# Kernel optimization log

Measured on AMD Instinct MI355X. Metric: run time of the kernel, lower is better.

The kernel has to match this reference:

```python
import jax, jax.numpy as jnp
import numpy as np

B, C, H, W, HEADS = 2, 128, 56, 56, 4
ASYM_W = 0.5


def setup_inputs() -> dict:
    key = jax.random.key(0)
    ks = jax.random.split(key, 9)
    s = lambda k, shape: jax.random.normal(k, shape, jnp.float32) * 0.02
    inner = C  # dim_head * heads == dim
    return {
        "x": jax.random.normal(ks[0], (B, C, H, W), jnp.float32),
        "Wq": s(ks[1], (inner, C)),
        "Wk": s(ks[2], (inner, C)),
        "Wv": s(ks[3], (inner, C)),
        "Wo": s(ks[4], (C, inner)),
        "bo": jnp.zeros((C,), jnp.float32),
        "Wa1": s(ks[5], (C, 2 * C)),
        "ba1": jnp.zeros((C,), jnp.float32),
        "Wa2": s(ks[6], (1, C)),
        "ba2": jnp.zeros((1,), jnp.float32),
    }


def _conv1x1(Wmat, t, bias=None):
    # 1x1 conv == per-pixel matmul over channels
    out = jnp.einsum('oc,bchw->bohw', Wmat, t)
    if bias is not None:
        out = out + bias[None, :, None, None]
    return out


def reference(x, Wq, Wk, Wv, Wo, bo, Wa1, ba1, Wa2, ba2):
    b, c, h, w = x.shape
    heads = HEADS
    dh = c // heads
    scale = dh ** -0.5

    # ---- asymmetry map ----
    left = x[:, :, :, : w // 2]
    right = x[:, :, :, w // 2:]
    right_flipped = right[:, :, :, ::-1]
    mw = min(left.shape[3], right_flipped.shape[3])
    cat = jnp.concatenate([left[:, :, :, :mw], right_flipped[:, :, :, :mw]], axis=1)
    a = _conv1x1(Wa1, cat, ba1)
    a = jax.nn.gelu(a, approximate=False)  # torch default GELU is exact erf
    a = _conv1x1(Wa2, a, ba2)
    a = jax.nn.sigmoid(a)
    # bilinear, align_corners=False == half-pixel convention of jax.image.resize
    asym = jax.image.resize(a, (b, 1, h, w), method='linear')

    # ---- q/k/v projections ----
    def heads_split(t):  # b (h d) x y -> b h (x y) d
        return t.reshape(b, heads, dh, h * w).transpose(0, 1, 3, 2)

    q = heads_split(_conv1x1(Wq, x))
    k = heads_split(_conv1x1(Wk, x))
    v = heads_split(_conv1x1(Wv, x))

    dots = jnp.einsum('bhid,bhjd->bhij', q, k) * scale  # [b,h,hw,hw]

    # 3x3 neighborhood mask, vectorized
    idx = jnp.arange(h * w)
    ii, jj = idx // w, idx % w
    mask = ((jnp.abs(ii[:, None] - ii[None, :]) <= 1)
            & (jnp.abs(jj[:, None] - jj[None, :]) <= 1)).astype(dots.dtype)
    dots = dots * mask + (1.0 - mask) * -1e9

    attn = jax.nn.softmax(dots, axis=-1)
    out = jnp.einsum('bhij,bhjd->bhid', attn, v)
    out = out.transpose(0, 1, 3, 2).reshape(b, c, h, w)  # b h (x y) d -> b (h d) x y

    out = out * (1.0 + ASYM_W * asym)
    return _conv1x1(Wo, out, bo)
```

## Files before the change

### kernel.cpp

```cpp
#include <hip/hip_runtime.h>
#include <hip/hip_bf16.h>
#include <math.h>

#define B_ 2
#define C_ 128
#define H_ 56
#define W_ 56
#define N_ (H_*W_)
#define HEADS_ 4
#define DH_ 32
#define MW_ 28
#define NPOS_ (H_*MW_)

typedef unsigned short ushort_t;
typedef __bf16 v8bf __attribute__((ext_vector_type(8)));
typedef float  v4f  __attribute__((ext_vector_type(4)));

#define MFMA16(a,b,c) __builtin_amdgcn_mfma_f32_16x16x32_bf16((a),(b),(c),0,0,0)

__device__ __forceinline__ unsigned short f2bf(float f) {
    return __builtin_bit_cast(unsigned short, __float2bfloat16(f));
}
__device__ __forceinline__ unsigned int bfpack(float a, float b) {
    return (unsigned int)f2bf(a) | ((unsigned int)f2bf(b) << 16);
}
__device__ __forceinline__ void unpack8(uint4 u, float* f) {
    f[0] = __uint_as_float(u.x << 16); f[1] = __uint_as_float(u.x & 0xffff0000u);
    f[2] = __uint_as_float(u.y << 16); f[3] = __uint_as_float(u.y & 0xffff0000u);
    f[4] = __uint_as_float(u.z << 16); f[5] = __uint_as_float(u.z & 0xffff0000u);
    f[6] = __uint_as_float(u.w << 16); f[7] = __uint_as_float(u.w & 0xffff0000u);
}

__global__ __launch_bounds__(256)
void xpose_kernel(const float* __restrict__ x, ushort_t* __restrict__ xbf) {
    __shared__ float xs[128 * 68];
    const int t  = threadIdx.x;
    const int n0 = blockIdx.x * 64;
    const int b  = blockIdx.y;
    const float* xb = x + (size_t)b * C_ * N_;

    for (int it = 0; it < 8; ++it) {
        int idx = t + it * 256;
        int c = idx >> 4, f4 = idx & 15;
        *(float4*)(&xs[c * 68 + f4 * 4]) =
            *(const float4*)(xb + (size_t)c * N_ + n0 + f4 * 4);
    }
    __syncthreads();
    const int rot = t & 7;
    for (int it = 0; it < 4; ++it) {
        int task = t + it * 256;
        int ug = task & 15, px = task >> 4;
        float f[8];
        #pragma unroll
        for (int s = 0; s < 8; ++s) {
            int u = (s + rot) & 7;
            f[u] = xs[(ug * 8 + u) * 68 + px];
        }
        uint4 o;
        o.x = bfpack(f[0], f[1]); o.y = bfpack(f[2], f[3]);
        o.z = bfpack(f[4], f[5]); o.w = bfpack(f[6], f[7]);
        *(uint4*)(xbf + ((size_t)b * N_ + n0 + px) * C_ + ug * 8) = o;
    }
}

__global__ __launch_bounds__(256)
void qkv_asym_kernel(const ushort_t* __restrict__ xbf,
                     const float* __restrict__ Wq, const float* __restrict__ Wk,
                     const float* __restrict__ Wv,
                     const float* __restrict__ Wa1, const float* __restrict__ ba1,
                     const float* __restrict__ Wa2, const float* __restrict__ ba2,
                     ushort_t* __restrict__ q, ushort_t* __restrict__ k,
                     ushort_t* __restrict__ v, float* __restrict__ aval) {
    __shared__ __align__(16) char smem[35840];
    const int t = threadIdx.x;
    const int b = blockIdx.z;
    const int wv_ = t >> 6;
    const int l   = t & 63;
    const int lr  = l & 15;
    const int lq  = l >> 4;

    if (blockIdx.y < 6) {
        ushort_t* WT = (ushort_t*)smem;
        ushort_t* XT = (ushort_t*)(smem + 17408);

        const int n0   = blockIdx.x * 64;
        const int mIdx = blockIdx.y >> 1;
        const int o0   = (blockIdx.y & 1) * 64;
        const float* W  = (mIdx == 0 ? Wq : (mIdx == 1 ? Wk : Wv));
        ushort_t* dst   = (mIdx == 0 ? q  : (mIdx == 1 ? k  : v ));

        for (int it = 0; it < 8; ++it) {
            int idx = t + it * 256;
            int row = idx >> 5, f4 = idx & 31;
            float4 w4 = *(const float4*)(W + (size_t)(o0 + row) * C_ + f4 * 4);
            ushort4 p4 = { f2bf(w4.x), f2bf(w4.y), f2bf(w4.z), f2bf(w4.w) };
            *(ushort4*)(WT + row * 136 + f4 * 4) = p4;
        }
        for (int it = 0; it < 4; ++it) {
            int idx = t + it * 256;
            int px = idx >> 4, g = idx & 15;
            uint4 r = *(const uint4*)(xbf + ((size_t)b * N_ + n0 + px) * C_ + g * 8);
            *(uint4*)(XT + px * 136 + g * 8) = r;
        }
        __syncthreads();

        v4f acc[4];
        #pragma unroll
        for (int nt = 0; nt < 4; ++nt) acc[nt] = (v4f){0.f, 0.f, 0.f, 0.f};

        #pragma unroll
        for (int ks = 0; ks < 4; ++ks) {
            v8bf af = *(const v8bf*)(WT + (wv_ * 16 + lr) * 136 + ks * 32 + lq * 8);
            #pragma unroll
            for (int nt = 0; nt < 4; ++nt) {
                v8bf bfr = *(const v8bf*)(XT + (nt * 16 + lr) * 136 + ks * 32 + lq * 8);
                acc[nt] = MFMA16(af, bfr, acc[nt]);
            }
        }

        __syncthreads();
        ushort_t* epT = WT;
        #pragma unroll
        for (int nt = 0; nt < 4; ++nt) {
            uint2 pk;
            pk.x = bfpack(acc[nt][0], acc[nt][1]);
            pk.y = bfpack(acc[nt][2], acc[nt][3]);
            *(uint2*)(epT + (nt * 16 + lr) * 136 + wv_ * 16 + lq * 4) = pk;
        }
        __syncthreads();
        for (int it = 0; it < 2; ++it) {
            int idx = t + it * 256;
            int px = idx >> 3, g = idx & 7;
            *(uint4*)(dst + ((size_t)b * N_ + n0 + px) * C_ + o0 + g * 8) =
                *(const uint4*)(epT + px * 136 + g * 8);
        }
    } else {
        ushort_t* wa  = (ushort_t*)smem;
        ushort_t* cat = (ushort_t*)(smem + 18432);
        float* wred   = (float*)(smem + 35328);

        const int P0 = blockIdx.x * 32;

        for (int it = 0; it < 4; ++it) {
            int idx = t + it * 256;
            int pos = idx >> 5, g = idx & 31;
            int pg = P0 + pos;
            int h = pg / MW_, j = pg - h * MW_;
            int n = h * W_ + ((g < 16) ? j : (W_ - 1 - j));
            uint4 r = *(const uint4*)(xbf + ((size_t)b * N_ + n) * C_ + (g & 15) * 8);
            *(uint4*)(cat + pos * 264 + g * 8) = r;
        }

        v4f acc2[2][2];
        #pragma unroll
        for (int mi = 0; mi < 2; ++mi)
            #pragma unroll
            for (int nt = 0; nt < 2; ++nt) acc2[mi][nt] = (v4f){0.f, 0.f, 0.f, 0.f};

        for (int kc = 0; kc < 4; ++kc) {
            __syncthreads();
            for (int it = 0; it < 8; ++it) {
                int idx = t + it * 256;
                int row = idx >> 4, f4 = idx & 15;
                float4 w4 = *(const float4*)(Wa1 + (size_t)row * 256 + kc * 64 + f4 * 4);
                ushort4 p4 = { f2bf(w4.x), f2bf(w4.y), f2bf(w4.z), f2bf(w4.w) };
                *(ushort4*)(wa + row * 72 + f4 * 4) = p4;
            }
            __syncthreads();
            #pragma unroll
            for (int ks = 0; ks < 2; ++ks) {
                v8bf a0f = *(const v8bf*)(wa + ((2*wv_ + 0) * 16 + lr) * 72 + ks * 32 + lq * 8);
                v8bf a1f = *(const v8bf*)(wa + ((2*wv_ + 1) * 16 + lr) * 72 + ks * 32 + lq * 8);
                v8bf b0f = *(const v8bf*)(cat + lr * 264        + kc * 64 + ks * 32 + lq * 8);
                v8bf b1f = *(const v8bf*)(cat + (16 + lr) * 264 + kc * 64 + ks * 32 + lq * 8);
                acc2[0][0] = MFMA16(a0f, b0f, acc2[0][0]);
                acc2[0][1] = MFMA16(a0f, b1f, acc2[0][1]);
                acc2[1][0] = MFMA16(a1f, b0f, acc2[1][0]);
                acc2[1][1] = MFMA16(a1f, b1f, acc2[1][1]);
            }
        }

        float p2[2] = {0.f, 0.f};
        #pragma unroll
        for (int mi = 0; mi < 2; ++mi) {
            #pragma unroll
            for (int r = 0; r < 4; ++r) {
                int m = (2*wv_ + mi) * 16 + lq * 4 + r;
                float wa2v = Wa2[m];
                float b1v  = ba1[m];
                #pragma unroll
                for (int nt = 0; nt < 2; ++nt) {
                    float val = acc2[mi][nt][r] + b1v;
                    float gl = 0.5f * val * (1.0f + erff(val * 0.7071067811865475f));
                    p2[nt] += gl * wa2v;
                }
            }
        }
        #pragma unroll
        for (int nt = 0; nt < 2; ++nt) {
            p2[nt] += __shfl_xor(p2[nt], 16, 64);
            p2[nt] += __shfl_xor(p2[nt], 32, 64);
        }
        if (l < 16) {
            wred[wv_ * 32 + lr]      = p2[0];
            wred[wv_ * 32 + 16 + lr] = p2[1];
        }
        __syncthreads();
        if (t < 32) {
            float s = wred[t] + wred[32 + t] + wred[64 + t] + wred[96 + t] + ba2[0];
            aval[(size_t)b * NPOS_ + P0 + t] = 1.0f / (1.0f + expf(-s));
        }
    }
}

__global__ __launch_bounds__(256)
void attn_oproj_kernel(const ushort_t* __restrict__ q, const ushort_t* __restrict__ k,
                       const ushort_t* __restrict__ v, const float* __restrict__ aval,
                       const float* __restrict__ Wo, const float* __restrict__ bo,
                       float* __restrict__ out) {
    __shared__ __align__(16) char smem[53248];
    ushort_t* WoT = (ushort_t*)smem;
    ushort_t* aoT = (ushort_t*)(smem + 34816);
    float*    ep  = (float*)(smem + 34816);

    const int t  = threadIdx.x;
    const int n0 = blockIdx.x * 32;
    const int b  = blockIdx.y;

    for (int it = 0; it < 16; ++it) {
        int idx = t + it * 256;
        int row = idx >> 5, f4 = idx & 31;
        float4 w4 = *(const float4*)(Wo + (size_t)row * C_ + f4 * 4);
        ushort4 p4 = { f2bf(w4.x), f2bf(w4.y), f2bf(w4.z), f2bf(w4.w) };
        *(ushort4*)(WoT + row * 136 + f4 * 4) = p4;
    }

    const size_t base = (size_t)b * N_ * C_;
    for (int u = 0; u < 2; ++u) {
        int task = t + u * 256;
        int s = task & 3, head = (task >> 2) & 3, p = task >> 4;
        int n = n0 + p;
        int i = n / W_, j = n - i * W_;
        int dbase = head * DH_ + s * 8;

        float qf[8];
        unpack8(*(const uint4*)(q + base + (size_t)n * C_ + dbase), qf);

        float dts[9]; int mm[9];
        #pragma unroll
        for (int tt = 0; tt < 9; ++tt) {
            int di = tt / 3 - 1, dj = tt % 3 - 1;
            int ii = i + di, jj = j + dj;
            bool ok = ((unsigned)ii < (unsigned)H_) && ((unsigned)jj < (unsigned)W_);
            int m = ok ? ii * W_ + jj : n;
            mm[tt] = m;
            float kf[8];
            unpack8(*(const uint4*)(k + base + (size_t)m * C_ + dbase), kf);
            float pd = qf[0]*kf[0] + qf[1]*kf[1] + qf[2]*kf[2] + qf[3]*kf[3]
                     + qf[4]*kf[4] + qf[5]*kf[5] + qf[6]*kf[6] + qf[7]*kf[7];
            pd += __shfl_xor(pd, 1, 64);
            pd += __shfl_xor(pd, 2, 64);
            dts[tt] = ok ? pd * 0.17677669529663687f : -1e30f;
        }
        float mx = dts[0];
        #pragma unroll
        for (int tt = 1; tt < 9; ++tt) mx = fmaxf(mx, dts[tt]);
        float sum = 0.f;
        #pragma unroll
        for (int tt = 0; tt < 9; ++tt) { dts[tt] = expf(dts[tt] - mx); sum += dts[tt]; }
        const float inv = 1.0f / sum;

        float acc[8] = {0,0,0,0,0,0,0,0};
        #pragma unroll
        for (int tt = 0; tt < 9; ++tt) {
            float vf[8];
            unpack8(*(const uint4*)(v + base + (size_t)mm[tt] * C_ + dbase), vf);
            float wt = dts[tt] * inv;
            #pragma unroll
            for (int d = 0; d < 8; ++d) acc[d] += wt * vf[d];
        }

        float f = 0.5f * (float)j - 0.25f;
        f = fminf(fmaxf(f, 0.0f), 27.0f);
        int i0 = (int)f; if (i0 > 26) i0 = 26;
        float frac = f - (float)i0;
        const float* av = aval + (size_t)b * NPOS_ + i * MW_;
        float a = av[i0] * (1.0f - frac) + av[i0 + 1] * frac;
        float sc = 1.0f + 0.5f * a;

        uint4 o;
        o.x = bfpack(acc[0] * sc, acc[1] * sc);
        o.y = bfpack(acc[2] * sc, acc[3] * sc);
        o.z = bfpack(acc[4] * sc, acc[5] * sc);
        o.w = bfpack(acc[6] * sc, acc[7] * sc);
        *(uint4*)(aoT + p * 136 + dbase) = o;
    }
    __syncthreads();

    const int wv_ = t >> 6, l = t & 63, lr = l & 15, lq = l >> 4;
    v4f acc4[2][2];
    #pragma unroll
    for (int mi = 0; mi < 2; ++mi)
        #pragma unroll
        for (int nt = 0; nt < 2; ++nt) acc4[mi][nt] = (v4f){0.f, 0.f, 0.f, 0.f};

    #pragma unroll
    for (int ks = 0; ks < 4; ++ks) {
        v8bf b0 = *(const v8bf*)(aoT + lr * 136        + ks * 32 + lq * 8);
        v8bf b1 = *(const v8bf*)(aoT + (16 + lr) * 136 + ks * 32 + lq * 8);
        #pragma unroll
        for (int mi = 0; mi < 2; ++mi) {
            v8bf af = *(const v8bf*)(WoT + ((wv_ * 2 + mi) * 16 + lr) * 136 + ks * 32 + lq * 8);
            acc4[mi][0] = MFMA16(af, b0, acc4[mi][0]);
            acc4[mi][1] = MFMA16(af, b1, acc4[mi][1]);
        }
    }
    __syncthreads();

    #pragma unroll
    for (int mi = 0; mi < 2; ++mi) {
        int o = (wv_ * 2 + mi) * 16 + lq * 4;
        float4 bv = *(const float4*)(bo + o);
        const float bvr[4] = { bv.x, bv.y, bv.z, bv.w };
        #pragma unroll
        for (int nt = 0; nt < 2; ++nt)
            #pragma unroll
            for (int r = 0; r < 4; ++r)
                ep[(o + r) * 36 + nt * 16 + lr] = acc4[mi][nt][r] + bvr[r];
    }
    __syncthreads();
    for (int it = 0; it < 4; ++it) {
        int idx = t + it * 256;
        int o = idx >> 3, f4 = idx & 7;
        *(float4*)(out + (size_t)b * C_ * N_ + (size_t)o * N_ + n0 + f4 * 4) =
            *(const float4*)(ep + o * 36 + f4 * 4);
    }
}

extern "C" void kernel_launch(void* const* d_in, const int* in_sizes, int n_in,
                              void* d_out, int out_size, void* d_ws, size_t ws_size,
                              hipStream_t stream) {
    const float* x   = (const float*)d_in[0];
    const float* Wq  = (const float*)d_in[1];
    const float* Wk  = (const float*)d_in[2];
    const float* Wv  = (const float*)d_in[3];
    const float* Wo  = (const float*)d_in[4];
    const float* bo  = (const float*)d_in[5];
    const float* Wa1 = (const float*)d_in[6];
    const float* ba1 = (const float*)d_in[7];
    const float* Wa2 = (const float*)d_in[8];
    const float* ba2 = (const float*)d_in[9];
    float* out = (float*)d_out;

    const size_t PXC = (size_t)B_ * N_ * C_;
    ushort_t* qb  = (ushort_t*)d_ws;
    ushort_t* kb  = qb + PXC;
    ushort_t* vb  = kb + PXC;
    ushort_t* xbf = vb + PXC;
    float*    aval = (float*)(xbf + PXC);

    xpose_kernel   <<<dim3(49, B_), 256, 0, stream>>>(x, xbf);
    qkv_asym_kernel<<<dim3(49, 7, B_), 256, 0, stream>>>(
        xbf, Wq, Wk, Wv, Wa1, ba1, Wa2, ba2, qb, kb, vb, aval);
    attn_oproj_kernel<<<dim3(98, B_), 256, 0, stream>>>(qb, kb, vb, aval, Wo, bo, out);
}
```

Before: 102.6 us.

## Fuse transpose into QKV/asym kernel and halve attention block pixel tile

```diff
diff --git a/kernel.cpp b/kernel.cpp
--- a/kernel.cpp
+++ b/kernel.cpp
@@ -32,39 +32,7 @@
 }
 
 __global__ __launch_bounds__(256)
-void xpose_kernel(const float* __restrict__ x, ushort_t* __restrict__ xbf) {
-    __shared__ float xs[128 * 68];
-    const int t  = threadIdx.x;
-    const int n0 = blockIdx.x * 64;
-    const int b  = blockIdx.y;
-    const float* xb = x + (size_t)b * C_ * N_;
-
-    for (int it = 0; it < 8; ++it) {
-        int idx = t + it * 256;
-        int c = idx >> 4, f4 = idx & 15;
-        *(float4*)(&xs[c * 68 + f4 * 4]) =
-            *(const float4*)(xb + (size_t)c * N_ + n0 + f4 * 4);
-    }
-    __syncthreads();
-    const int rot = t & 7;
-    for (int it = 0; it < 4; ++it) {
-        int task = t + it * 256;
-        int ug = task & 15, px = task >> 4;
-        float f[8];
-        #pragma unroll
-        for (int s = 0; s < 8; ++s) {
-            int u = (s + rot) & 7;
-            f[u] = xs[(ug * 8 + u) * 68 + px];
-        }
-        uint4 o;
-        o.x = bfpack(f[0], f[1]); o.y = bfpack(f[2], f[3]);
-        o.z = bfpack(f[4], f[5]); o.w = bfpack(f[6], f[7]);
-        *(uint4*)(xbf + ((size_t)b * N_ + n0 + px) * C_ + ug * 8) = o;
-    }
-}
-
-__global__ __launch_bounds__(256)
-void qkv_asym_kernel(const ushort_t* __restrict__ xbf,
+void qkv_asym_kernel(const float* __restrict__ x,
                      const float* __restrict__ Wq, const float* __restrict__ Wk,
                      const float* __restrict__ Wv,
                      const float* __restrict__ Wa1, const float* __restrict__ ba1,
@@ -88,6 +56,7 @@
         const int o0   = (blockIdx.y & 1) * 64;
         const float* W  = (mIdx == 0 ? Wq : (mIdx == 1 ? Wk : Wv));
         ushort_t* dst   = (mIdx == 0 ? q  : (mIdx == 1 ? k  : v ));
+        const float* xb = x + (size_t)b * C_ * N_;
 
         for (int it = 0; it < 8; ++it) {
             int idx = t + it * 256;
@@ -96,11 +65,18 @@
             ushort4 p4 = { f2bf(w4.x), f2bf(w4.y), f2bf(w4.z), f2bf(w4.w) };
             *(ushort4*)(WT + row * 136 + f4 * 4) = p4;
         }
-        for (int it = 0; it < 4; ++it) {
-            int idx = t + it * 256;
-            int px = idx >> 4, g = idx & 15;
-            uint4 r = *(const uint4*)(xbf + ((size_t)b * N_ + n0 + px) * C_ + g * 8);
-            *(uint4*)(XT + px * 136 + g * 8) = r;
+        {
+            int px = t & 63, g = t >> 6;
+            const float* xc = xb + n0 + px;
+            for (int it = 0; it < 8; ++it) {
+                int c0 = (g + it * 4) * 4;
+                float a0 = xc[(size_t)(c0 + 0) * N_];
+                float a1 = xc[(size_t)(c0 + 1) * N_];
+                float a2 = xc[(size_t)(c0 + 2) * N_];
+                float a3 = xc[(size_t)(c0 + 3) * N_];
+                ushort4 p4 = { f2bf(a0), f2bf(a1), f2bf(a2), f2bf(a3) };
+                *(ushort4*)(XT + px * 136 + c0) = p4;
+            }
         }
         __syncthreads();
 
@@ -140,15 +116,23 @@
         float* wred   = (float*)(smem + 35328);
 
         const int P0 = blockIdx.x * 32;
-
-        for (int it = 0; it < 4; ++it) {
-            int idx = t + it * 256;
-            int pos = idx >> 5, g = idx & 31;
+        const float* xb = x + (size_t)b * C_ * N_;
+
+        {
+            int pos = t & 31, chg = t >> 5;
             int pg = P0 + pos;
             int h = pg / MW_, j = pg - h * MW_;
-            int n = h * W_ + ((g < 16) ? j : (W_ - 1 - j));
-            uint4 r = *(const uint4*)(xbf + ((size_t)b * N_ + n) * C_ + (g & 15) * 8);
-            *(uint4*)(cat + pos * 264 + g * 8) = r;
+            int col = (chg < 4) ? (h * W_ + j) : (h * W_ + (W_ - 1 - j));
+            int cbase = (chg & 3) * 32;
+            const float* src = xb + col;
+            ushort_t* crow = cat + pos * 264 + chg * 32;
+            #pragma unroll
+            for (int u = 0; u < 16; ++u) {
+                float f0 = src[(size_t)(cbase + 2 * u) * N_];
+                float f1 = src[(size_t)(cbase + 2 * u + 1) * N_];
+                ushort2 pp = { f2bf(f0), f2bf(f1) };
+                *(ushort2*)(crow + 2 * u) = pp;
+            }
         }
 
         v4f acc2[2][2];
@@ -218,13 +202,13 @@
                        const ushort_t* __restrict__ v, const float* __restrict__ aval,
                        const float* __restrict__ Wo, const float* __restrict__ bo,
                        float* __restrict__ out) {
-    __shared__ __align__(16) char smem[53248];
+    __shared__ __align__(16) char smem[45056];
     ushort_t* WoT = (ushort_t*)smem;
     ushort_t* aoT = (ushort_t*)(smem + 34816);
     float*    ep  = (float*)(smem + 34816);
 
     const int t  = threadIdx.x;
-    const int n0 = blockIdx.x * 32;
+    const int n0 = blockIdx.x * 16;
     const int b  = blockIdx.y;
 
     for (int it = 0; it < 16; ++it) {
@@ -236,9 +220,8 @@
     }
 
     const size_t base = (size_t)b * N_ * C_;
-    for (int u = 0; u < 2; ++u) {
-        int task = t + u * 256;
-        int s = task & 3, head = (task >> 2) & 3, p = task >> 4;
+    {
+        int s = t & 3, head = (t >> 2) & 3, p = t >> 4;
         int n = n0 + p;
         int i = n / W_, j = n - i * W_;
         int dbase = head * DH_ + s * 8;
@@ -298,21 +281,17 @@
     __syncthreads();
 
     const int wv_ = t >> 6, l = t & 63, lr = l & 15, lq = l >> 4;
-    v4f acc4[2][2];
-    #pragma unroll
-    for (int mi = 0; mi < 2; ++mi)
-        #pragma unroll
-        for (int nt = 0; nt < 2; ++nt) acc4[mi][nt] = (v4f){0.f, 0.f, 0.f, 0.f};
+    v4f acc4[2];
+    acc4[0] = (v4f){0.f, 0.f, 0.f, 0.f};
+    acc4[1] = (v4f){0.f, 0.f, 0.f, 0.f};
 
     #pragma unroll
     for (int ks = 0; ks < 4; ++ks) {
-        v8bf b0 = *(const v8bf*)(aoT + lr * 136        + ks * 32 + lq * 8);
-        v8bf b1 = *(const v8bf*)(aoT + (16 + lr) * 136 + ks * 32 + lq * 8);
+        v8bf b0 = *(const v8bf*)(aoT + lr * 136 + ks * 32 + lq * 8);
         #pragma unroll
         for (int mi = 0; mi < 2; ++mi) {
             v8bf af = *(const v8bf*)(WoT + ((wv_ * 2 + mi) * 16 + lr) * 136 + ks * 32 + lq * 8);
-            acc4[mi][0] = MFMA16(af, b0, acc4[mi][0]);
-            acc4[mi][1] = MFMA16(af, b1, acc4[mi][1]);
+            acc4[mi] = MFMA16(af, b0, acc4[mi]);
         }
     }
     __syncthreads();
@@ -323,17 +302,15 @@
         float4 bv = *(const float4*)(bo + o);
         const float bvr[4] = { bv.x, bv.y, bv.z, bv.w };
         #pragma unroll
-        for (int nt = 0; nt < 2; ++nt)
-            #pragma unroll
-            for (int r = 0; r < 4; ++r)
-                ep[(o + r) * 36 + nt * 16 + lr] = acc4[mi][nt][r] + bvr[r];
+        for (int r = 0; r < 4; ++r)
+            ep[(o + r) * 20 + lr] = acc4[mi][r] + bvr[r];
     }
     __syncthreads();
-    for (int it = 0; it < 4; ++it) {
+    for (int it = 0; it < 2; ++it) {
         int idx = t + it * 256;
-        int o = idx >> 3, f4 = idx & 7;
+        int o = idx >> 2, f4 = idx & 3;
         *(float4*)(out + (size_t)b * C_ * N_ + (size_t)o * N_ + n0 + f4 * 4) =
-            *(const float4*)(ep + o * 36 + f4 * 4);
+            *(const float4*)(ep + o * 20 + f4 * 4);
     }
 }
 
@@ -356,11 +333,9 @@
     ushort_t* qb  = (ushort_t*)d_ws;
     ushort_t* kb  = qb + PXC;
     ushort_t* vb  = kb + PXC;
-    ushort_t* xbf = vb + PXC;
-    float*    aval = (float*)(xbf + PXC);
-
-    xpose_kernel   <<<dim3(49, B_), 256, 0, stream>>>(x, xbf);
+    float*    aval = (float*)(vb + PXC);
+
     qkv_asym_kernel<<<dim3(49, 7, B_), 256, 0, stream>>>(
-        xbf, Wq, Wk, Wv, Wa1, ba1, Wa2, ba2, qb, kb, vb, aval);
-    attn_oproj_kernel<<<dim3(98, B_), 256, 0, stream>>>(qb, kb, vb, aval, Wo, bo, out);
-}
+        x, Wq, Wk, Wv, Wa1, ba1, Wa2, ba2, qb, kb, vb, aval);
+    attn_oproj_kernel<<<dim3(196, B_), 256, 0, stream>>>(qb, kb, vb, aval, Wo, bo, out);
+}
```

Measured after the change: 89.34 us. 1.15x faster.
